# Kernel tuning notes

Measured on AMD Instinct MI355X. Metric: run time of the kernel, lower is better.

Reference implementation:

```python
import jax, jax.numpy as jnp
import numpy as np

# Module hyperparameters (match init_kwargs)
T0, Z0, T1, Z1, K, S, ROUTING = 4, 16, 8, 16, 5, 1, 3
PAD = 2  # hard-coded padding=2 in the torch module
N, H, W_SP = 4, 128, 128


def setup_inputs() -> dict:
    key = jax.random.key(0)
    k1, k2 = jax.random.split(key)
    u = jax.random.normal(k1, (N, T0, Z0, H, W_SP), dtype=jnp.float32)
    # t_0 independent Conv2d(z_0 -> t_1*z_1, k, s, padding=2, bias=False) weights
    W = jax.random.normal(k2, (T0, T1 * Z1, Z0, K, K), dtype=jnp.float32) * 0.05
    return {"u": u, "W": W}


def _squash(p):
    # squash along last (z_1) axis, matching torch: p_norm = sqrt(|p|^2 + 1e-9)
    n2 = jnp.sum(p * p, axis=-1, keepdims=True)
    n = jnp.sqrt(n2 + 1e-9)
    return n2 / (1.0 + n2) * p / n


def _capsule_convs(u, W):
    # t_0 independent convs == one grouped conv with feature_group_count=t_0
    n, t0, z0, h, w = u.shape
    x = u.reshape(n, t0 * z0, h, w)
    wk = W.reshape(t0 * T1 * Z1, z0, K, K)
    y = jax.lax.conv_general_dilated(
        x, wk, window_strides=(S, S), padding=[(PAD, PAD), (PAD, PAD)],
        dimension_numbers=("NCHW", "OIHW", "NCHW"), feature_group_count=t0)
    h1, w1 = y.shape[2], y.shape[3]
    # [N, t0*t1*z1, H1, W1] -> u_hat [t0, N, H1, W1, t1, z1]
    y = y.reshape(n, t0, T1, Z1, h1, w1)
    return jnp.transpose(y, (1, 0, 4, 5, 2, 3))


def _routing(u_hat):
    t0, n, h, w, t1, z1 = u_hat.shape
    dt = u_hat.dtype
    b = jnp.zeros((t0, n, t1, h, w), dt)  # NCHW layout per capsule type
    neg_inf = jnp.array(-jnp.inf, dt)
    zero = jnp.array(0.0, dt)
    win = (1, 1, 1, K, K)
    ones = (1, 1, 1, 1, 1)
    pad = [(0, 0), (0, 0), (0, 0), (PAD, PAD), (PAD, PAD)]
    v = None
    for d in range(ROUTING):
        uh = jax.lax.stop_gradient(u_hat) if d < ROUTING - 1 else u_hat
        # stability max: max_pool2d(k,1,pad=2) (pads with -inf) then max over t1
        b_max = jax.lax.reduce_window(b, neg_inf, jax.lax.max, win, ones, pad)
        b_max = jnp.max(b_max, axis=2, keepdims=True)
        c = jnp.exp(b - b_max)  # [t0, N, t1, H, W]
        # conv2d_same with ones kernel [1,t1,k,k] == channel-sum then kxk box-sum
        sum_c = jax.lax.reduce_window(jnp.sum(c, axis=2, keepdims=True), zero,
                                      jax.lax.add, win, ones, pad)
        r = c / sum_c                                   # [t0, N, t1, H, W]
        r = jnp.transpose(r, (0, 1, 3, 4, 2))[..., None]  # [t0,N,H,W,t1,1]
        p = jnp.sum(r * uh, axis=0)                     # [N, H, W, t1, z1]
        v = _squash(p)
        # NOTE: the original torch code computes b + (u_hat*v).sum(4) into a
        # list `b_t_list_` that is never assigned back, so b stays zero across
        # iterations. We faithfully reproduce that (no b update).
    return jnp.transpose(v, (0, 3, 4, 1, 2))  # [N, t1, z1, H, W]


def reference(u, W):
    return _routing(_capsule_convs(u, W))
```

## Files before the change

### kernel.cpp

```cpp
#include <hip/hip_runtime.h>
#include <hip/hip_bf16.h>


#define CO 128

typedef __attribute__((ext_vector_type(8))) short bf16x8;
typedef __attribute__((ext_vector_type(4))) float f32x4;

__global__ __launch_bounds__(256) void k_reorder(const float* __restrict__ Wsrc,
                                                 ushort* __restrict__ Wr2) {
    int idx = blockIdx.x * 256 + threadIdx.x;
    if (idx >= 25 * 128 * 64) return;
    int ci = idx & 63;
    int r  = idx >> 6;
    int co = r & 127;
    int kk = r >> 7;
    int t0 = ci >> 4, z0 = ci & 15;
    __hip_bfloat16 b = __float2bfloat16(Wsrc[((t0 * CO + co) * 16 + z0) * 25 + kk]);
    Wr2[idx] = *(ushort*)&b;
}

__global__ __launch_bounds__(256) void k_pre(const float* __restrict__ u,
                                             ushort* __restrict__ ut) {
    __shared__ float lt[64][65];
    int b = blockIdx.x;
    int wc = b & 1; int nh = b >> 1; int h = nh & 127; int n = nh >> 7;
    int w0 = wc * 64;
    int t = threadIdx.x;
    int w = t & 63; int cg = t >> 6;
    const float* up = u + (size_t)n * (64 * 128 * 128) + h * 128 + w0 + w;
#pragma unroll
    for (int i = 0; i < 16; ++i) {
        int ci = cg * 16 + i;
        lt[w][ci] = up[(size_t)ci * (128 * 128)];
    }
    __syncthreads();
    int ci2 = t & 63; int pg = t >> 6;
    ushort* op = ut + (((size_t)(n * 128 + h)) * 128 + w0) * 64 + ci2;
#pragma unroll
    for (int i = 0; i < 16; ++i) {
        int w2 = pg * 16 + i;
        __hip_bfloat16 bv = __float2bfloat16(lt[w2][ci2]);
        op[(size_t)w2 * 64] = *(ushort*)&bv;
    }
}

__global__ __launch_bounds__(256) void k_caps(const ushort* __restrict__ ut,
                                              const ushort* __restrict__ Wr2,
                                              float* __restrict__ out) {
    __shared__ ushort As[240 * 80];
    __shared__ ushort Bs[128 * 80];

    int tid = threadIdx.x;
    int bid = blockIdx.x;
    int bx = bid & 7, by = (bid >> 3) & 15, n = bid >> 7;
    int h0 = by * 8, w0 = bx * 16;

    for (int i = tid; i < 1920; i += 256) {
        int p = i >> 3, c = i & 7;
        int rr = p / 20, cc = p - rr * 20;
        int hh = h0 + rr - 2, ww = w0 + cc - 2;
        bf16x8 v = {};
        if ((unsigned)hh < 128u && (unsigned)ww < 128u)
            v = *(const bf16x8*)(ut + (((size_t)(n * 128 + hh)) * 128 + ww) * 64 + c * 8);
        *(bf16x8*)&As[p * 80 + c * 8] = v;
    }

    int lane = tid & 63, wid = tid >> 6;
    int wm4  = (wid >> 1) * 4;
    int wn64 = (wid & 1) * 64;
    int q = lane >> 4, m16 = lane & 15;

    f32x4 acc[4][4] = {};

    bf16x8 pre[4];
#pragma unroll
    for (int j = 0; j < 4; ++j)
        pre[j] = *(const bf16x8*)(Wr2 + (size_t)(tid + j * 256) * 8);

    int aBase = (wm4 * 20 + m16) * 80 + q * 8;
    int bBase = (wn64 + m16) * 80 + q * 8;

#pragma unroll
    for (int kk = 0; kk < 25; ++kk) {
        const int kh = kk / 5, kw = kk % 5;
        __syncthreads();
#pragma unroll
        for (int j = 0; j < 4; ++j) {
            int i = tid + j * 256;
            *(bf16x8*)&Bs[(i >> 3) * 80 + (i & 7) * 8] = pre[j];
        }
        __syncthreads();
        if (kk < 24) {
#pragma unroll
            for (int j = 0; j < 4; ++j)
                pre[j] = *(const bf16x8*)(Wr2 + (size_t)(kk + 1) * 8192 + (tid + j * 256) * 8);
        }
#pragma unroll
        for (int ks = 0; ks < 2; ++ks) {
            bf16x8 a[4], bb[4];
#pragma unroll
            for (int mi = 0; mi < 4; ++mi)
                a[mi] = *(const bf16x8*)&As[aBase + ((mi + kh) * 20 + kw) * 80 + ks * 32];
#pragma unroll
            for (int ni = 0; ni < 4; ++ni)
                bb[ni] = *(const bf16x8*)&Bs[bBase + ni * (16 * 80) + ks * 32];
#pragma unroll
            for (int mi = 0; mi < 4; ++mi)
#pragma unroll
                for (int ni = 0; ni < 4; ++ni)
                    acc[mi][ni] = __builtin_amdgcn_mfma_f32_16x16x32_bf16(
                        a[mi], bb[ni], acc[mi][ni], 0, 0, 0);
        }
    }

#pragma unroll
    for (int mi = 0; mi < 4; ++mi) {
        int h = h0 + wm4 + mi;
        int hlo = h - 2; if (hlo < 0) hlo = 0;
        int hhi = h + 2; if (hhi > 127) hhi = 127;
        float cnth = (float)(hhi - hlo + 1);
#pragma unroll
        for (int ni = 0; ni < 4; ++ni) {
            f32x4 cv = acc[mi][ni];
            float ov[4];
#pragma unroll
            for (int reg = 0; reg < 4; ++reg) {
                int w = w0 + q * 4 + reg;
                int wlo = w - 2; if (wlo < 0) wlo = 0;
                int whi = w + 2; if (whi > 127) whi = 127;
                float s = 1.f / (8.f * cnth * (float)(whi - wlo + 1));
                float pv = cv[reg] * s;
                float n2 = pv * pv;
                n2 += __shfl_xor(n2, 1);
                n2 += __shfl_xor(n2, 2);
                n2 += __shfl_xor(n2, 4);
                n2 += __shfl_xor(n2, 8);
                float fac = n2 / ((1.f + n2) * sqrtf(n2 + 1e-9f));
                ov[reg] = pv * fac;
            }
            int co = wn64 + ni * 16 + m16;
            *(float4*)(out + (((size_t)(n * CO + co)) << 14) + h * 128 + w0 + q * 4) =
                make_float4(ov[0], ov[1], ov[2], ov[3]);
        }
    }
}

extern "C" void kernel_launch(void* const* d_in, const int* in_sizes, int n_in,
                              void* d_out, int out_size, void* d_ws, size_t ws_size,
                              hipStream_t stream) {
    const float* u    = (const float*)d_in[0];
    const float* Wsrc = (const float*)d_in[1];
    float* out = (float*)d_out;
    ushort* Wr2 = (ushort*)d_ws;
    ushort* ut  = (ushort*)((char*)d_ws + 409600);

    k_reorder<<<800, 256, 0, stream>>>(Wsrc, Wr2);
    k_pre<<<1024, 256, 0, stream>>>(u, ut);
    k_caps<<<512, 256, 0, stream>>>(ut, Wr2, out);
}
```

Baseline: 109.1 us.

## Load conv weights directly to registers, reorder loop for A reuse, fuse reorder kernel

The weight-reorder kernel is merged into the input transpose kernel as extra blocks, removing one launch. The main conv kernel no longer stages weights through LDS with two barriers per tap. Each lane instead loads its B fragments straight from global memory into registers, with a two-step prefetch. The tap loop is reordered by kw so eight A rows are loaded from LDS once and reused across the five kh taps. The costs are higher register pressure (launch bounds set to 2 blocks per SM) and a dependence on global or L2 latency for the B loads.

```diff
diff --git a/kernel.cpp b/kernel.cpp
--- a/kernel.cpp
+++ b/kernel.cpp
@@ -7,26 +7,30 @@
 typedef __attribute__((ext_vector_type(8))) short bf16x8;
 typedef __attribute__((ext_vector_type(4))) float f32x4;
 
-__global__ __launch_bounds__(256) void k_reorder(const float* __restrict__ Wsrc,
-                                                 ushort* __restrict__ Wr2) {
-    int idx = blockIdx.x * 256 + threadIdx.x;
-    if (idx >= 25 * 128 * 64) return;
-    int ci = idx & 63;
-    int r  = idx >> 6;
-    int co = r & 127;
-    int kk = r >> 7;
-    int t0 = ci >> 4, z0 = ci & 15;
-    __hip_bfloat16 b = __float2bfloat16(Wsrc[((t0 * CO + co) * 16 + z0) * 25 + kk]);
-    Wr2[idx] = *(ushort*)&b;
-}
-
 __global__ __launch_bounds__(256) void k_pre(const float* __restrict__ u,
-                                             ushort* __restrict__ ut) {
+                                             const float* __restrict__ Wsrc,
+                                             ushort* __restrict__ ut,
+                                             ushort* __restrict__ Wr2) {
+    int b = blockIdx.x;
+    int t = threadIdx.x;
+    if (b >= 1024) {
+        int base = (b - 1024) * 2048 + t;
+#pragma unroll
+        for (int j = 0; j < 8; ++j) {
+            int idx = base + j * 256;
+            int ci = idx & 63;
+            int r  = idx >> 6;
+            int co = r & 127;
+            int kk = r >> 7;
+            int t0 = ci >> 4, z0 = ci & 15;
+            __hip_bfloat16 bb = __float2bfloat16(Wsrc[((t0 * CO + co) * 16 + z0) * 25 + kk]);
+            Wr2[idx] = *(ushort*)&bb;
+        }
+        return;
+    }
     __shared__ float lt[64][65];
-    int b = blockIdx.x;
     int wc = b & 1; int nh = b >> 1; int h = nh & 127; int n = nh >> 7;
     int w0 = wc * 64;
-    int t = threadIdx.x;
     int w = t & 63; int cg = t >> 6;
     const float* up = u + (size_t)n * (64 * 128 * 128) + h * 128 + w0 + w;
 #pragma unroll
@@ -45,16 +49,29 @@
     }
 }
 
-__global__ __launch_bounds__(256) void k_caps(const ushort* __restrict__ ut,
-                                              const ushort* __restrict__ Wr2,
-                                              float* __restrict__ out) {
+__global__ __launch_bounds__(256, 2) void k_caps(const ushort* __restrict__ ut,
+                                                 const ushort* __restrict__ Wr2,
+                                                 float* __restrict__ out) {
     __shared__ ushort As[240 * 80];
-    __shared__ ushort Bs[128 * 80];
 
     int tid = threadIdx.x;
     int bid = blockIdx.x;
     int bx = bid & 7, by = (bid >> 3) & 15, n = bid >> 7;
     int h0 = by * 8, w0 = bx * 16;
+
+    int lane = tid & 63, wid = tid >> 6;
+    int wm4  = (wid >> 1) * 4;
+    int wn64 = (wid & 1) * 64;
+    int q = lane >> 4, m16 = lane & 15;
+
+    const ushort* bpb = Wr2 + (wn64 + m16) * 64 + q * 8;
+
+    bf16x8 bn1[4], bn2[4];
+#pragma unroll
+    for (int ni = 0; ni < 4; ++ni) {
+        bn1[ni] = *(const bf16x8*)(bpb + ni * 1024);
+        bn2[ni] = *(const bf16x8*)(bpb + 5 * 8192 + ni * 1024);
+    }
 
     for (int i = tid; i < 1920; i += 256) {
         int p = i >> 3, c = i & 7;
@@ -65,52 +82,40 @@
             v = *(const bf16x8*)(ut + (((size_t)(n * 128 + hh)) * 128 + ww) * 64 + c * 8);
         *(bf16x8*)&As[p * 80 + c * 8] = v;
     }
-
-    int lane = tid & 63, wid = tid >> 6;
-    int wm4  = (wid >> 1) * 4;
-    int wn64 = (wid & 1) * 64;
-    int q = lane >> 4, m16 = lane & 15;
+    __syncthreads();
 
     f32x4 acc[4][4] = {};
-
-    bf16x8 pre[4];
-#pragma unroll
-    for (int j = 0; j < 4; ++j)
-        pre[j] = *(const bf16x8*)(Wr2 + (size_t)(tid + j * 256) * 8);
-
     int aBase = (wm4 * 20 + m16) * 80 + q * 8;
-    int bBase = (wn64 + m16) * 80 + q * 8;
 
 #pragma unroll
-    for (int kk = 0; kk < 25; ++kk) {
-        const int kh = kk / 5, kw = kk % 5;
-        __syncthreads();
-#pragma unroll
-        for (int j = 0; j < 4; ++j) {
-            int i = tid + j * 256;
-            *(bf16x8*)&Bs[(i >> 3) * 80 + (i & 7) * 8] = pre[j];
-        }
-        __syncthreads();
-        if (kk < 24) {
-#pragma unroll
-            for (int j = 0; j < 4; ++j)
-                pre[j] = *(const bf16x8*)(Wr2 + (size_t)(kk + 1) * 8192 + (tid + j * 256) * 8);
-        }
+    for (int kw = 0; kw < 5; ++kw) {
 #pragma unroll
         for (int ks = 0; ks < 2; ++ks) {
-            bf16x8 a[4], bb[4];
+            bf16x8 a[8];
 #pragma unroll
-            for (int mi = 0; mi < 4; ++mi)
-                a[mi] = *(const bf16x8*)&As[aBase + ((mi + kh) * 20 + kw) * 80 + ks * 32];
+            for (int r = 0; r < 8; ++r)
+                a[r] = *(const bf16x8*)&As[aBase + (r * 20 + kw) * 80 + ks * 32];
 #pragma unroll
-            for (int ni = 0; ni < 4; ++ni)
-                bb[ni] = *(const bf16x8*)&Bs[bBase + ni * (16 * 80) + ks * 32];
+            for (int kh = 0; kh < 5; ++kh) {
+                const int s = kw * 10 + ks * 5 + kh;
+                bf16x8 bc[4];
 #pragma unroll
-            for (int mi = 0; mi < 4; ++mi)
+                for (int ni = 0; ni < 4; ++ni) { bc[ni] = bn1[ni]; bn1[ni] = bn2[ni]; }
+                const int s2 = s + 2;
+                if (s2 < 50) {
+                    const int kw2 = s2 / 10, ks2 = (s2 / 5) & 1, kh2 = s2 % 5;
+                    const int off2 = (kh2 * 5 + kw2) * 8192 + ks2 * 32;
 #pragma unroll
-                for (int ni = 0; ni < 4; ++ni)
-                    acc[mi][ni] = __builtin_amdgcn_mfma_f32_16x16x32_bf16(
-                        a[mi], bb[ni], acc[mi][ni], 0, 0, 0);
+                    for (int ni = 0; ni < 4; ++ni)
+                        bn2[ni] = *(const bf16x8*)(bpb + off2 + ni * 1024);
+                }
+#pragma unroll
+                for (int mi = 0; mi < 4; ++mi)
+#pragma unroll
+                    for (int ni = 0; ni < 4; ++ni)
+                        acc[mi][ni] = __builtin_amdgcn_mfma_f32_16x16x32_bf16(
+                            a[mi + kh], bc[ni], acc[mi][ni], 0, 0, 0);
+            }
         }
     }
 
@@ -155,7 +160,6 @@
     ushort* Wr2 = (ushort*)d_ws;
     ushort* ut  = (ushort*)((char*)d_ws + 409600);
 
-    k_reorder<<<800, 256, 0, stream>>>(Wsrc, Wr2);
-    k_pre<<<1024, 256, 0, stream>>>(u, ut);
+    k_pre<<<1124, 256, 0, stream>>>(u, Wsrc, ut, Wr2);
     k_caps<<<512, 256, 0, stream>>>(ut, Wr2, out);
 }
```

Result: slower. 133.2 us (+22.1%).
